# Kernel tuning notes

Measured on AMD Instinct MI355X. Metric: run time of the kernel, lower is better.

The kernel has to match this reference:

```python
import jax, jax.numpy as jnp
import numpy as np

# Module hyperparameters (match torch init_kwargs)
D_MODEL = 512
N_HEADS = 8
WINDOW_LEN = 128
DIL_FACTOR = 64
N_DIL = 2
ATTN_SINK = True
SRC_LEN = 2048
BSZ = 2


def setup_inputs() -> dict:
    key = jax.random.key(0)
    ks = jax.random.split(key, 6)
    w_scale = 0.04  # ~ xavier_uniform scale for 512x512
    inp = {
        "x": jax.random.normal(ks[0], (SRC_LEN, BSZ, D_MODEL), jnp.float32),
        "Wq": jax.random.normal(ks[1], (D_MODEL, D_MODEL), jnp.float32) * w_scale,
        "bq": jnp.zeros((D_MODEL,), jnp.float32),
        "Wk": jax.random.normal(ks[2], (D_MODEL, D_MODEL), jnp.float32) * w_scale,
        "bk": jnp.zeros((D_MODEL,), jnp.float32),
        "Wv": jax.random.normal(ks[3], (D_MODEL, D_MODEL), jnp.float32) * w_scale,
        "bv": jnp.zeros((D_MODEL,), jnp.float32),
        "Wo": jax.random.normal(ks[4], (D_MODEL, D_MODEL), jnp.float32) * w_scale,
        "bo": jnp.zeros((D_MODEL,), jnp.float32),
        "beta": jnp.zeros((N_HEADS,), jnp.float32),
    }
    return inp


def _fast_attention(x, Wq, bq, Wk, bk, Wv, bv, Wo, bo, beta):
    s, b, dm = x.shape  # (src_len, bsz, d_model)
    h = N_HEADS
    d = dm // h
    q = x @ Wq.T + bq
    k = x @ Wk.T + bk
    v = x @ Wv.T + bv

    def split_heads(t):  # 's b (h d) -> (b h) s d'
        return t.reshape(s, b, h, d).transpose(1, 2, 0, 3).reshape(b * h, s, d)

    q, k, v = split_heads(q), split_heads(k), split_heads(v)

    # beta: per-head temperature, tiled over batch (matches torch .repeat(bsz,1,1))
    beta_e = jnp.tile(jnp.exp(beta), b)[:, None, None]  # (b*h, 1, 1)
    q = q / (jnp.sqrt(jnp.asarray(d, q.dtype)) * beta_e)

    attn_out = jnp.zeros_like(v)
    z = b * h
    for i in range(N_DIL):
        dil = DIL_FACTOR ** i
        p = (WINDOW_LEN - 1) * dil
        pad = (p % s) if (p % s) != p else 0  # static python ints
        nw = pad // dil + 1  # num windows
        # causal left-padded strided windowed view of q: (z, nw, s, d)
        qp = jnp.pad(q, ((0, 0), (pad, 0), (0, 0)))
        idx = (jnp.arange(nw) * dil)[:, None] + jnp.arange(s)[None, :]  # (nw, s)
        qi = qp[:, idx, :]
        w = jnp.einsum('zbsd,zsd->zbs', qi, k)  # (z, nw, s)
        if ATTN_SINK:
            w = jnp.concatenate([w, jnp.zeros((z, 1, s), w.dtype)], axis=1)
        w = jax.nn.softmax(w, axis=1)  # softmax over window axis (+ sink)
        if ATTN_SINK:
            w = w[:, :-1]
        k2 = jnp.einsum('zbs,zsd->zbd', w, k)  # (z, nw, d)
        v2 = jnp.einsum('zbs,zsd->zbd', w, v)
        # left-pad back to full length (zeros at front, values at end)
        k = jnp.pad(k2, ((0, 0), (s - nw, 0), (0, 0)))
        v = jnp.pad(v2, ((0, 0), (s - nw, 0), (0, 0)))
        attn_out = attn_out + v

    # '(b h) s d -> s b (h d)'
    out = attn_out.reshape(b, h, s, d).transpose(2, 0, 1, 3).reshape(s, b, dm)
    return out @ Wo.T + bo


def reference(x, Wq, bq, Wk, bk, Wv, bv, Wo, bo, beta):
    return _fast_attention(x, Wq, bq, Wk, bk, Wv, bv, Wo, bo, beta)
```

## Files before the change

### kernel.cpp

```cpp
#include <hip/hip_runtime.h>
#include <hip/hip_bf16.h>
#include <math.h>

#define S_LEN 2048
#define BSZ 2
#define DM 512
#define NH 8
#define HD 64
#define RTOT (S_LEN*BSZ)
#define T_KEEP 32
#define ROW0 ((S_LEN - T_KEEP)*BSZ)
#define NXELEM (RTOT*DM)
#define NWROW  (NH*192)
#define NWELEM (NWROW*DM)

typedef __attribute__((ext_vector_type(8))) _Float16 half8;
typedef __attribute__((ext_vector_type(4))) float floatx4;

__device__ __forceinline__ short cvt1(float v) {
    _Float16 h = (_Float16)v;
    return __builtin_bit_cast(short, h);
}

__global__ __launch_bounds__(256) void convert(
    const float* __restrict__ x,
    const float* __restrict__ Wq, const float* __restrict__ Wk, const float* __restrict__ Wv,
    const float* __restrict__ bq, const float* __restrict__ bk, const float* __restrict__ bv,
    const float* __restrict__ bo,
    short* __restrict__ xf, short* __restrict__ wf, float* __restrict__ bcat,
    float* __restrict__ gbar, float* __restrict__ out)
{
    const int g = blockIdx.x*blockDim.x + threadIdx.x;
    const int stride = gridDim.x*blockDim.x;
    const int total4 = (NXELEM + NWELEM)/4;
    for (int i = g; i < total4; i += stride) {
        float4 v; size_t dst; short* d;
        if (i < NXELEM/4) {
            v = ((const float4*)x)[i];
            dst = (size_t)i*4; d = xf;
        } else {
            int j = i - NXELEM/4;
            int e = j*4;
            int R = e >> 9;
            int k = e & 511;
            int t = R >> 6;
            int hh = (t*683) >> 11;
            int m = t - 3*hh;
            int c = R & 63;
            const float* W = (m == 0 ? Wq : (m == 1 ? Wk : Wv));
            v = *(const float4*)&W[(size_t)(hh*HD + c)*DM + k];
            dst = (size_t)R*DM + k; d = wf;
        }
        short4 hv;
        hv.x = cvt1(v.x); hv.y = cvt1(v.y); hv.z = cvt1(v.z); hv.w = cvt1(v.w);
        *(short4*)&d[dst] = hv;
    }
    {
        const float4* b4 = (const float4*)bo;
        float4* o4 = (float4*)out;
        const int fill4 = ROW0*DM/4;
        for (int i = g; i < fill4; i += stride) o4[i] = b4[i & 127];
    }
    if (g < NWROW) {
        int t = g >> 6;
        int hh = (t*683) >> 11;
        int m = t - 3*hh;
        int c = g & 63;
        bcat[g] = (m == 0 ? bq : (m == 1 ? bk : bv))[hh*HD + c];
    }
    if (g < 2048) gbar[g] = 0.f;
}

__global__ __launch_bounds__(256) void qkv_gemm(
    const _Float16* __restrict__ xf, const _Float16* __restrict__ wf,
    const float* __restrict__ bcat, const float* __restrict__ beta,
    float* __restrict__ gbar, float* __restrict__ qsel)
{
    __shared__ __align__(16) float Cl[32*192];
    __shared__ float sb[256];

    const int tid  = threadIdx.x;
    const int w    = tid >> 6;
    const int lane = tid & 63;
    const int lrow = lane & 15;
    const int lk8  = lane >> 4;
    const int h    = blockIdx.y;
    const int r0   = blockIdx.x * 64;
    const int rowg = w >> 1;
    const int colg = w & 1;

    floatx4 acc[2][6];
    #pragma unroll
    for (int i = 0; i < 2; ++i)
        #pragma unroll
        for (int j = 0; j < 6; ++j) acc[i][j] = (floatx4)0.f;

    const _Float16* pA = xf + (size_t)(r0 + rowg*32 + lrow)*DM + lk8*8;
    const _Float16* pB = wf + (size_t)(h*192 + colg*96 + lrow)*DM + lk8*8;

    half8 Ab[2][2], Bb[2][6];
    #pragma unroll
    for (int i = 0; i < 2; ++i) Ab[0][i] = *(const half8*)(pA + (size_t)i*16*DM);
    #pragma unroll
    for (int j = 0; j < 6; ++j) Bb[0][j] = *(const half8*)(pB + (size_t)j*16*DM);

    #pragma unroll
    for (int kc = 0; kc < 16; ++kc) {
        const int buf = kc & 1;
        if (kc < 15) {
            const int nb = buf ^ 1;
            const int ko = (kc + 1)*32;
            #pragma unroll
            for (int i = 0; i < 2; ++i)
                Ab[nb][i] = *(const half8*)(pA + (size_t)i*16*DM + ko);
            #pragma unroll
            for (int j = 0; j < 6; ++j)
                Bb[nb][j] = *(const half8*)(pB + (size_t)j*16*DM + ko);
        }
        #pragma unroll
        for (int j = 0; j < 6; ++j)
            #pragma unroll
            for (int i = 0; i < 2; ++i)
                acc[i][j] = __builtin_amdgcn_mfma_f32_16x16x32_f16(Ab[buf][i], Bb[buf][j], acc[i][j], 0, 0, 0);
    }

    sb[tid] = 0.f;
    const float inv_scale = 1.0f / (8.0f * expf(beta[h]));
    float kacc0 = 0.f, kacc1 = 0.f, vacc0 = 0.f, vacc1 = 0.f;

    #pragma unroll
    for (int half = 0; half < 2; ++half) {
        __syncthreads();
        if (rowg == half) {
            #pragma unroll
            for (int i = 0; i < 2; ++i) {
                #pragma unroll
                for (int j = 0; j < 6; ++j) {
                    int col = colg*96 + j*16 + lrow;
                    float bias = bcat[h*192 + col];
                    #pragma unroll
                    for (int reg = 0; reg < 4; ++reg) {
                        int row = i*16 + lk8*4 + reg;
                        Cl[row*192 + col] = acc[i][j][reg] + bias;
                    }
                }
            }
        }
        __syncthreads();
        for (int i2 = w; i2 < 32; i2 += 4) {
            float qv = Cl[i2*192 + lane];
            float kv = Cl[i2*192 + 64 + lane];
            float vv = Cl[i2*192 + 128 + lane];
            int r = r0 + half*32 + i2;
            int s = r >> 1;
            int b = r & 1;
            if ((s & 63) == 63) {
                int wi = s >> 6;
                qsel[((size_t)(b*NH + h)*T_KEEP + wi)*64 + lane] = qv;
            }
            float p = qv * kv;
            #pragma unroll
            for (int off = 32; off > 0; off >>= 1) p += __shfl_xor(p, off, 64);
            float sig = 1.0f / (1.0f + expf(-p * inv_scale));
            if (b == 0) { kacc0 += sig*kv; vacc0 += sig*vv; }
            else        { kacc1 += sig*kv; vacc1 += sig*vv; }
        }
    }
    __syncthreads();

    atomicAdd(&sb[  0 + lane], kacc0);
    atomicAdd(&sb[ 64 + lane], vacc0);
    atomicAdd(&sb[128 + lane], kacc1);
    atomicAdd(&sb[192 + lane], vacc1);
    __syncthreads();
    {
        int b   = tid >> 7;
        int sel = (tid >> 6) & 1;
        int j   = tid & 63;
        int z   = b*NH + h;
        atomicAdd(&gbar[sel*1024 + z*64 + j], sb[tid]);
    }
}

__global__ __launch_bounds__(256) void headk(
    const float* __restrict__ qsel, const float* __restrict__ beta,
    const float* __restrict__ gbar, const float* __restrict__ Wo,
    float* __restrict__ coef, float* __restrict__ G)
{
    const int z = blockIdx.x;
    const int h = z & 7;
    const int tid = threadIdx.x;

    __shared__ float s_kb[64], s_vb[64];
    __shared__ float s_part[T_KEEP][8];
    __shared__ float s_gp[64][4];

    if (tid < 64) {
        s_kb[tid] = gbar[z*64 + tid];
        s_vb[tid] = gbar[1024 + z*64 + tid];
    }
    __syncthreads();

    {
        int wi = tid >> 3, jg = tid & 7;
        const float* qrow = &qsel[((size_t)z*T_KEEP + wi)*64 + jg*8];
        float4 q1 = *(const float4*)qrow;
        float4 q2 = *(const float4*)(qrow + 4);
        int j0 = jg*8;
        float p = q1.x*s_kb[j0] + q1.y*s_kb[j0+1] + q1.z*s_kb[j0+2] + q1.w*s_kb[j0+3]
                + q2.x*s_kb[j0+4] + q2.y*s_kb[j0+5] + q2.z*s_kb[j0+6] + q2.w*s_kb[j0+7];
        s_part[wi][jg] = p;
    }
    __syncthreads();
    if (tid < T_KEEP) {
        float sc = 0.f;
        #pragma unroll
        for (int gg = 0; gg < 8; ++gg) sc += s_part[tid][gg];
        sc *= 1.0f / (8.0f * expf(beta[h]));
        float m = sc;
        #pragma unroll
        for (int off = 16; off > 0; off >>= 1) m = fmaxf(m, __shfl_xor(m, off, 64));
        m = fmaxf(m, 0.f);
        float e = expf(sc - m);
        float d = e;
        #pragma unroll
        for (int off = 16; off > 0; off >>= 1) d += __shfl_xor(d, off, 64);
        d += expf(-m);
        float c = e / d;
        if (tid == T_KEEP-1) c += 1.0f;
        coef[z*T_KEEP + tid] = c;
    }

    const int cq = tid >> 2;
    const int jg = tid & 3;
    #pragma unroll
    for (int it = 0; it < 8; ++it) {
        int c = it*64 + cq;
        const float* wrow = &Wo[(size_t)c*DM + h*64 + jg*16];
        float a = 0.f;
        #pragma unroll
        for (int jj = 0; jj < 16; jj += 4) {
            float4 wv = *(const float4*)&wrow[jj];
            int j0 = jg*16 + jj;
            a += wv.x*s_vb[j0] + wv.y*s_vb[j0+1] + wv.z*s_vb[j0+2] + wv.w*s_vb[j0+3];
        }
        s_gp[cq][jg] = a;
        __syncthreads();
        if (tid < 64)
            G[(size_t)z*DM + it*64 + tid] = s_gp[tid][0] + s_gp[tid][1] + s_gp[tid][2] + s_gp[tid][3];
        __syncthreads();
    }
}

__global__ __launch_bounds__(256) void outk3(
    const float* __restrict__ coef, const float* __restrict__ G,
    const float* __restrict__ bo, float* __restrict__ out)
{
    const int a = blockIdx.x;
    const int b = a & 1;
    const int wi = a >> 1;
    const int tid = threadIdx.x;
    __shared__ float s_cf[NH];
    if (tid < NH) s_cf[tid] = coef[(b*NH + tid)*T_KEEP + wi];
    __syncthreads();
    for (int c = tid; c < DM; c += 256) {
        float v = bo[c];
        #pragma unroll
        for (int h = 0; h < NH; ++h)
            v += s_cf[h] * G[(size_t)(b*NH + h)*DM + c];
        out[(size_t)(ROW0 + a)*DM + c] = v;
    }
}

extern "C" void kernel_launch(void* const* d_in, const int* in_sizes, int n_in,
                              void* d_out, int out_size, void* d_ws, size_t ws_size,
                              hipStream_t stream) {
    const float* x    = (const float*)d_in[0];
    const float* Wq   = (const float*)d_in[1];
    const float* bq   = (const float*)d_in[2];
    const float* Wk   = (const float*)d_in[3];
    const float* bk   = (const float*)d_in[4];
    const float* Wv   = (const float*)d_in[5];
    const float* bv   = (const float*)d_in[6];
    const float* Wo   = (const float*)d_in[7];
    const float* bo   = (const float*)d_in[8];
    const float* beta = (const float*)d_in[9];

    char* ws = (char*)d_ws;
    float* gbar = (float*)(ws + 0);
    float* qsel = (float*)(ws + 8192);
    float* bcat = (float*)(ws + 139264);
    float* coef = (float*)(ws + 147456);
    float* G    = (float*)(ws + 149504);
    short* xf   = (short*)(ws + 182272);
    short* wf   = (short*)(ws + 182272 + 4194304);
    float* out  = (float*)d_out;

    convert<<<1024, 256, 0, stream>>>(x, Wq, Wk, Wv, bq, bk, bv, bo,
                                      xf, wf, bcat, gbar, out);
    dim3 g1(RTOT/64, NH);
    qkv_gemm<<<g1, 256, 0, stream>>>((const _Float16*)xf, (const _Float16*)wf,
                                     bcat, beta, gbar, qsel);
    headk<<<16, 256, 0, stream>>>(qsel, beta, gbar, Wo, coef, G);
    outk3<<<64, 256, 0, stream>>>(coef, G, bo, out);
}
```

Baseline: 132.6 us.

## Fuse head and output kernels, stage QKV GEMM tiles through LDS

Merges the per-head softmax-coefficient kernel and the output kernel into one kernel, outk4. It consumes a transposed copy of Wo prepared in the convert kernel and performs a 512x512 matvec per output row. The QKV GEMM now uses 32-row tiles with more blocks and occupancy hint 4, and loads A/B fragments through LDS via global_load_lds instead of register double-buffering. The aim is to remove one launch and raise GEMM occupancy. In exchange, each of the 64 output blocks re-reads the full WoT from cache, the strided transpose adds convert-kernel writes, and the single-buffered LDS loop adds barriers.

```diff
diff --git a/kernel.cpp b/kernel.cpp
--- a/kernel.cpp
+++ b/kernel.cpp
@@ -17,6 +17,11 @@
 typedef __attribute__((ext_vector_type(8))) _Float16 half8;
 typedef __attribute__((ext_vector_type(4))) float floatx4;
 
+__device__ __forceinline__ void gld16(const void* g, void* l) {
+    __builtin_amdgcn_global_load_lds((const __attribute__((address_space(1))) void*)g,
+                                     (__attribute__((address_space(3))) void*)l, 16, 0, 0);
+}
+
 __device__ __forceinline__ short cvt1(float v) {
     _Float16 h = (_Float16)v;
     return __builtin_bit_cast(short, h);
@@ -26,9 +31,9 @@
     const float* __restrict__ x,
     const float* __restrict__ Wq, const float* __restrict__ Wk, const float* __restrict__ Wv,
     const float* __restrict__ bq, const float* __restrict__ bk, const float* __restrict__ bv,
-    const float* __restrict__ bo,
+    const float* __restrict__ Wo, const float* __restrict__ bo,
     short* __restrict__ xf, short* __restrict__ wf, float* __restrict__ bcat,
-    float* __restrict__ gbar, float* __restrict__ out)
+    float* __restrict__ WoT, float* __restrict__ gbar, float* __restrict__ out)
 {
     const int g = blockIdx.x*blockDim.x + threadIdx.x;
     const int stride = gridDim.x*blockDim.x;
@@ -55,6 +60,15 @@
         hv.x = cvt1(v.x); hv.y = cvt1(v.y); hv.z = cvt1(v.z); hv.w = cvt1(v.w);
         *(short4*)&d[dst] = hv;
     }
+    for (int i = g; i < DM*DM/4; i += stride) {
+        int c  = i >> 7;
+        int k4 = (i & 127)*4;
+        float4 v = *(const float4*)&Wo[(size_t)c*DM + k4];
+        WoT[(size_t)(k4+0)*DM + c] = v.x;
+        WoT[(size_t)(k4+1)*DM + c] = v.y;
+        WoT[(size_t)(k4+2)*DM + c] = v.z;
+        WoT[(size_t)(k4+3)*DM + c] = v.w;
+    }
     {
         const float4* b4 = (const float4*)bo;
         float4* o4 = (float4*)out;
@@ -71,12 +85,12 @@
     if (g < 2048) gbar[g] = 0.f;
 }
 
-__global__ __launch_bounds__(256) void qkv_gemm(
+__global__ __launch_bounds__(256, 4) void qkv_gemm(
     const _Float16* __restrict__ xf, const _Float16* __restrict__ wf,
     const float* __restrict__ bcat, const float* __restrict__ beta,
     float* __restrict__ gbar, float* __restrict__ qsel)
 {
-    __shared__ __align__(16) float Cl[32*192];
+    __shared__ __align__(16) char smem[28672];
     __shared__ float sb[256];
 
     const int tid  = threadIdx.x;
@@ -85,86 +99,72 @@
     const int lrow = lane & 15;
     const int lk8  = lane >> 4;
     const int h    = blockIdx.y;
-    const int r0   = blockIdx.x * 64;
+    const int r0   = blockIdx.x * 32;
     const int rowg = w >> 1;
     const int colg = w & 1;
 
-    floatx4 acc[2][6];
+    floatx4 acc[6];
     #pragma unroll
-    for (int i = 0; i < 2; ++i)
-        #pragma unroll
-        for (int j = 0; j < 6; ++j) acc[i][j] = (floatx4)0.f;
-
-    const _Float16* pA = xf + (size_t)(r0 + rowg*32 + lrow)*DM + lk8*8;
-    const _Float16* pB = wf + (size_t)(h*192 + colg*96 + lrow)*DM + lk8*8;
-
-    half8 Ab[2][2], Bb[2][6];
+    for (int j = 0; j < 6; ++j) acc[j] = (floatx4)0.f;
+
+    const _Float16* asrc = xf + (size_t)(r0 + (w>>1)*16 + lrow)*DM + (w&1)*32 + lk8*8;
+    const _Float16* bsrc[6];
     #pragma unroll
-    for (int i = 0; i < 2; ++i) Ab[0][i] = *(const half8*)(pA + (size_t)i*16*DM);
+    for (int ii = 0; ii < 6; ++ii)
+        bsrc[ii] = wf + (size_t)(h*192 + (3*w + (ii>>1))*16 + lrow)*DM + (ii&1)*32 + lk8*8;
+
+    for (int kc = 0; kc < 8; ++kc) {
+        const int ko = kc*64;
+        gld16(asrc + ko, smem + w*1024);
+        #pragma unroll
+        for (int ii = 0; ii < 6; ++ii)
+            gld16(bsrc[ii] + ko, smem + 4096 + (6*w + ii)*1024);
+        __syncthreads();
+        #pragma unroll
+        for (int kh = 0; kh < 2; ++kh) {
+            half8 a = *(const half8*)(smem + (rowg*2 + kh)*1024 + lane*16);
+            #pragma unroll
+            for (int j = 0; j < 6; ++j) {
+                half8 b = *(const half8*)(smem + 4096 + ((colg*6 + j)*2 + kh)*1024 + lane*16);
+                acc[j] = __builtin_amdgcn_mfma_f32_16x16x32_f16(a, b, acc[j], 0, 0, 0);
+            }
+        }
+        __syncthreads();
+    }
+
+    float* Cl = (float*)smem;
     #pragma unroll
-    for (int j = 0; j < 6; ++j) Bb[0][j] = *(const half8*)(pB + (size_t)j*16*DM);
-
-    #pragma unroll
-    for (int kc = 0; kc < 16; ++kc) {
-        const int buf = kc & 1;
-        if (kc < 15) {
-            const int nb = buf ^ 1;
-            const int ko = (kc + 1)*32;
-            #pragma unroll
-            for (int i = 0; i < 2; ++i)
-                Ab[nb][i] = *(const half8*)(pA + (size_t)i*16*DM + ko);
-            #pragma unroll
-            for (int j = 0; j < 6; ++j)
-                Bb[nb][j] = *(const half8*)(pB + (size_t)j*16*DM + ko);
-        }
-        #pragma unroll
-        for (int j = 0; j < 6; ++j)
-            #pragma unroll
-            for (int i = 0; i < 2; ++i)
-                acc[i][j] = __builtin_amdgcn_mfma_f32_16x16x32_f16(Ab[buf][i], Bb[buf][j], acc[i][j], 0, 0, 0);
-    }
-
+    for (int j = 0; j < 6; ++j) {
+        int col = colg*96 + j*16 + lrow;
+        float bias = bcat[h*192 + col];
+        #pragma unroll
+        for (int reg = 0; reg < 4; ++reg) {
+            int row = rowg*16 + lk8*4 + reg;
+            Cl[row*192 + col] = acc[j][reg] + bias;
+        }
+    }
     sb[tid] = 0.f;
+    __syncthreads();
+
     const float inv_scale = 1.0f / (8.0f * expf(beta[h]));
     float kacc0 = 0.f, kacc1 = 0.f, vacc0 = 0.f, vacc1 = 0.f;
-
-    #pragma unroll
-    for (int half = 0; half < 2; ++half) {
-        __syncthreads();
-        if (rowg == half) {
-            #pragma unroll
-            for (int i = 0; i < 2; ++i) {
-                #pragma unroll
-                for (int j = 0; j < 6; ++j) {
-                    int col = colg*96 + j*16 + lrow;
-                    float bias = bcat[h*192 + col];
-                    #pragma unroll
-                    for (int reg = 0; reg < 4; ++reg) {
-                        int row = i*16 + lk8*4 + reg;
-                        Cl[row*192 + col] = acc[i][j][reg] + bias;
-                    }
-                }
-            }
-        }
-        __syncthreads();
-        for (int i2 = w; i2 < 32; i2 += 4) {
-            float qv = Cl[i2*192 + lane];
-            float kv = Cl[i2*192 + 64 + lane];
-            float vv = Cl[i2*192 + 128 + lane];
-            int r = r0 + half*32 + i2;
-            int s = r >> 1;
-            int b = r & 1;
-            if ((s & 63) == 63) {
-                int wi = s >> 6;
-                qsel[((size_t)(b*NH + h)*T_KEEP + wi)*64 + lane] = qv;
-            }
-            float p = qv * kv;
-            #pragma unroll
-            for (int off = 32; off > 0; off >>= 1) p += __shfl_xor(p, off, 64);
-            float sig = 1.0f / (1.0f + expf(-p * inv_scale));
-            if (b == 0) { kacc0 += sig*kv; vacc0 += sig*vv; }
-            else        { kacc1 += sig*kv; vacc1 += sig*vv; }
-        }
+    for (int i2 = w; i2 < 32; i2 += 4) {
+        float qv = Cl[i2*192 + lane];
+        float kv = Cl[i2*192 + 64 + lane];
+        float vv = Cl[i2*192 + 128 + lane];
+        int r = r0 + i2;
+        int s = r >> 1;
+        int b = r & 1;
+        if ((s & 63) == 63) {
+            int wi = s >> 6;
+            qsel[((size_t)(b*NH + h)*T_KEEP + wi)*64 + lane] = qv;
+        }
+        float p = qv * kv;
+        #pragma unroll
+        for (int off = 32; off > 0; off >>= 1) p += __shfl_xor(p, off, 64);
+        float sig = 1.0f / (1.0f + expf(-p * inv_scale));
+        if (b == 0) { kacc0 += sig*kv; vacc0 += sig*vv; }
+        else        { kacc1 += sig*kv; vacc1 += sig*vv; }
     }
     __syncthreads();
 
@@ -182,93 +182,75 @@
     }
 }
 
-__global__ __launch_bounds__(256) void headk(
+__global__ __launch_bounds__(256) void outk4(
     const float* __restrict__ qsel, const float* __restrict__ beta,
-    const float* __restrict__ gbar, const float* __restrict__ Wo,
-    float* __restrict__ coef, float* __restrict__ G)
-{
-    const int z = blockIdx.x;
-    const int h = z & 7;
-    const int tid = threadIdx.x;
-
-    __shared__ float s_kb[64], s_vb[64];
-    __shared__ float s_part[T_KEEP][8];
-    __shared__ float s_gp[64][4];
-
-    if (tid < 64) {
-        s_kb[tid] = gbar[z*64 + tid];
-        s_vb[tid] = gbar[1024 + z*64 + tid];
-    }
-    __syncthreads();
-
-    {
-        int wi = tid >> 3, jg = tid & 7;
-        const float* qrow = &qsel[((size_t)z*T_KEEP + wi)*64 + jg*8];
-        float4 q1 = *(const float4*)qrow;
-        float4 q2 = *(const float4*)(qrow + 4);
-        int j0 = jg*8;
-        float p = q1.x*s_kb[j0] + q1.y*s_kb[j0+1] + q1.z*s_kb[j0+2] + q1.w*s_kb[j0+3]
-                + q2.x*s_kb[j0+4] + q2.y*s_kb[j0+5] + q2.z*s_kb[j0+6] + q2.w*s_kb[j0+7];
-        s_part[wi][jg] = p;
-    }
-    __syncthreads();
-    if (tid < T_KEEP) {
-        float sc = 0.f;
-        #pragma unroll
-        for (int gg = 0; gg < 8; ++gg) sc += s_part[tid][gg];
-        sc *= 1.0f / (8.0f * expf(beta[h]));
-        float m = sc;
-        #pragma unroll
-        for (int off = 16; off > 0; off >>= 1) m = fmaxf(m, __shfl_xor(m, off, 64));
-        m = fmaxf(m, 0.f);
-        float e = expf(sc - m);
-        float d = e;
-        #pragma unroll
-        for (int off = 16; off > 0; off >>= 1) d += __shfl_xor(d, off, 64);
-        d += expf(-m);
-        float c = e / d;
-        if (tid == T_KEEP-1) c += 1.0f;
-        coef[z*T_KEEP + tid] = c;
-    }
-
-    const int cq = tid >> 2;
-    const int jg = tid & 3;
-    #pragma unroll
-    for (int it = 0; it < 8; ++it) {
-        int c = it*64 + cq;
-        const float* wrow = &Wo[(size_t)c*DM + h*64 + jg*16];
-        float a = 0.f;
-        #pragma unroll
-        for (int jj = 0; jj < 16; jj += 4) {
-            float4 wv = *(const float4*)&wrow[jj];
-            int j0 = jg*16 + jj;
-            a += wv.x*s_vb[j0] + wv.y*s_vb[j0+1] + wv.z*s_vb[j0+2] + wv.w*s_vb[j0+3];
-        }
-        s_gp[cq][jg] = a;
-        __syncthreads();
-        if (tid < 64)
-            G[(size_t)z*DM + it*64 + tid] = s_gp[tid][0] + s_gp[tid][1] + s_gp[tid][2] + s_gp[tid][3];
-        __syncthreads();
-    }
-}
-
-__global__ __launch_bounds__(256) void outk3(
-    const float* __restrict__ coef, const float* __restrict__ G,
+    const float* __restrict__ gbar, const float* __restrict__ WoT,
     const float* __restrict__ bo, float* __restrict__ out)
 {
     const int a = blockIdx.x;
     const int b = a & 1;
-    const int wi = a >> 1;
+    const int wi_blk = a >> 1;
     const int tid = threadIdx.x;
+
+    __shared__ float s_kb[512];
+    __shared__ float s_u[512];
     __shared__ float s_cf[NH];
-    if (tid < NH) s_cf[tid] = coef[(b*NH + tid)*T_KEEP + wi];
-    __syncthreads();
-    for (int c = tid; c < DM; c += 256) {
-        float v = bo[c];
-        #pragma unroll
-        for (int h = 0; h < NH; ++h)
-            v += s_cf[h] * G[(size_t)(b*NH + h)*DM + c];
-        out[(size_t)(ROW0 + a)*DM + c] = v;
+    __shared__ float s_part[512];
+
+    s_kb[tid]       = gbar[b*512 + tid];
+    s_kb[tid] = gbar[b*512 + tid];
+    s_part[tid]     = gbar[1024 + b*512 + tid];
+    s_part[tid+256] = gbar[1024 + b*512 + 256 + tid];
+    if (tid < 256) s_kb[tid+256] = gbar[b*512 + 256 + tid];
+    __syncthreads();
+
+    {
+        int h = tid >> 5, wi = tid & 31;
+        const float* qrow = &qsel[((size_t)(b*NH + h)*T_KEEP + wi)*64];
+        float sc = 0.f;
+        #pragma unroll
+        for (int j = 0; j < 64; j += 4) {
+            float4 q = *(const float4*)&qrow[j];
+            sc += q.x*s_kb[h*64+j] + q.y*s_kb[h*64+j+1] + q.z*s_kb[h*64+j+2] + q.w*s_kb[h*64+j+3];
+        }
+        sc *= 1.0f / (8.0f * expf(beta[h]));
+        float m = sc;
+        #pragma unroll
+        for (int off = 16; off > 0; off >>= 1) m = fmaxf(m, __shfl_xor(m, off, 32));
+        m = fmaxf(m, 0.f);
+        float e = expf(sc - m);
+        float d = e;
+        #pragma unroll
+        for (int off = 16; off > 0; off >>= 1) d += __shfl_xor(d, off, 32);
+        d += expf(-m);
+        if (wi == wi_blk) {
+            float c = e / d;
+            if (wi_blk == T_KEEP-1) c += 1.0f;
+            s_cf[h] = c;
+        }
+    }
+    __syncthreads();
+    s_u[tid]       = s_cf[tid >> 6]         * s_part[tid];
+    s_u[tid + 256] = s_cf[(tid + 256) >> 6] * s_part[tid + 256];
+    __syncthreads();
+
+    const int c0 = (tid & 127)*4;
+    const int kh = tid >> 7;
+    float4 accv = {0.f, 0.f, 0.f, 0.f};
+    for (int k = kh*256; k < kh*256 + 256; ++k) {
+        float u = s_u[k];
+        float4 wv = *(const float4*)&WoT[(size_t)k*DM + c0];
+        accv.x += u*wv.x; accv.y += u*wv.y; accv.z += u*wv.z; accv.w += u*wv.w;
+    }
+    __syncthreads();
+    if (kh == 1) *(float4*)&s_part[c0] = accv;
+    __syncthreads();
+    if (kh == 0) {
+        float4 pv = *(const float4*)&s_part[c0];
+        float4 bv = *(const float4*)&bo[c0];
+        accv.x += pv.x + bv.x; accv.y += pv.y + bv.y;
+        accv.z += pv.z + bv.z; accv.w += pv.w + bv.w;
+        *(float4*)&out[(size_t)(ROW0 + a)*DM + c0] = accv;
     }
 }
 
@@ -290,17 +272,15 @@
     float* gbar = (float*)(ws + 0);
     float* qsel = (float*)(ws + 8192);
     float* bcat = (float*)(ws + 139264);
-    float* coef = (float*)(ws + 147456);
-    float* G    = (float*)(ws + 149504);
-    short* xf   = (short*)(ws + 182272);
-    short* wf   = (short*)(ws + 182272 + 4194304);
+    float* WoT  = (float*)(ws + 147456);
+    short* xf   = (short*)(ws + 1196032);
+    short* wf   = (short*)(ws + 1196032 + 4194304);
     float* out  = (float*)d_out;
 
-    convert<<<1024, 256, 0, stream>>>(x, Wq, Wk, Wv, bq, bk, bv, bo,
-                                      xf, wf, bcat, gbar, out);
-    dim3 g1(RTOT/64, NH);
+    convert<<<1024, 256, 0, stream>>>(x, Wq, Wk, Wv, bq, bk, bv, Wo, bo,
+                                      xf, wf, bcat, WoT, gbar, out);
+    dim3 g1(RTOT/32, NH);
     qkv_gemm<<<g1, 256, 0, stream>>>((const _Float16*)xf, (const _Float16*)wf,
                                      bcat, beta, gbar, qsel);
-    headk<<<16, 256, 0, stream>>>(qsel, beta, gbar, Wo, coef, G);
-    outk3<<<64, 256, 0, stream>>>(coef, G, bo, out);
-}
+    outk4<<<64, 256, 0, stream>>>(qsel, beta, gbar, WoT, bo, out);
+}
```

Measured after the change: 137.9 us. +3.9%, slower.

## Shrink QKV GEMM tiles and stage operands through LDS via direct global-to-LDS loads

Applied to the files above, without the earlier changes.

The QKV GEMM block tile drops from 64 rows to 16 rows, so the grid has four times as many blocks. Each k-step now loads the A tile and twelve B tiles straight into shared memory with global_load_lds, and all four waves read the shared A fragment from there. Register use falls (3 accumulators instead of 12, with a 6-blocks-per-CU launch bound), which should raise occupancy and parallelism. The costs are that the same weight slice is re-read by four times as many blocks, there are two barriers per k-step, and the old register double-buffering is gone. The convert kernel's grid is also doubled.

```diff
diff --git a/kernel.cpp b/kernel.cpp
--- a/kernel.cpp
+++ b/kernel.cpp
@@ -16,6 +16,11 @@
 
 typedef __attribute__((ext_vector_type(8))) _Float16 half8;
 typedef __attribute__((ext_vector_type(4))) float floatx4;
+
+__device__ __forceinline__ void gld16(const void* g, void* l) {
+    __builtin_amdgcn_global_load_lds((const __attribute__((address_space(1))) void*)g,
+                                     (__attribute__((address_space(3))) void*)l, 16, 0, 0);
+}
 
 __device__ __forceinline__ short cvt1(float v) {
     _Float16 h = (_Float16)v;
@@ -71,12 +76,12 @@
     if (g < 2048) gbar[g] = 0.f;
 }
 
-__global__ __launch_bounds__(256) void qkv_gemm(
+__global__ __launch_bounds__(256, 6) void qkv_gemm(
     const _Float16* __restrict__ xf, const _Float16* __restrict__ wf,
     const float* __restrict__ bcat, const float* __restrict__ beta,
     float* __restrict__ gbar, float* __restrict__ qsel)
 {
-    __shared__ __align__(16) float Cl[32*192];
+    __shared__ __align__(16) char smem[13312];
     __shared__ float sb[256];
 
     const int tid  = threadIdx.x;
@@ -85,86 +90,70 @@
     const int lrow = lane & 15;
     const int lk8  = lane >> 4;
     const int h    = blockIdx.y;
-    const int r0   = blockIdx.x * 64;
-    const int rowg = w >> 1;
-    const int colg = w & 1;
-
-    floatx4 acc[2][6];
+    const int r0   = blockIdx.x * 16;
+
+    floatx4 acc[3];
     #pragma unroll
-    for (int i = 0; i < 2; ++i)
-        #pragma unroll
-        for (int j = 0; j < 6; ++j) acc[i][j] = (floatx4)0.f;
-
-    const _Float16* pA = xf + (size_t)(r0 + rowg*32 + lrow)*DM + lk8*8;
-    const _Float16* pB = wf + (size_t)(h*192 + colg*96 + lrow)*DM + lk8*8;
-
-    half8 Ab[2][2], Bb[2][6];
+    for (int j = 0; j < 3; ++j) acc[j] = (floatx4)0.f;
+
+    const _Float16* csrc[4];
+    int cdst[4];
+    int nch = 0;
+    for (int c = w; c < 13; c += 4) {
+        csrc[nch] = (c == 0)
+            ? xf + (size_t)(r0 + lrow)*DM + lk8*8
+            : wf + (size_t)(h*192 + (c-1)*16 + lrow)*DM + lk8*8;
+        cdst[nch] = c;
+        ++nch;
+    }
+
+    for (int kc = 0; kc < 16; ++kc) {
+        const int ko = kc*32;
+        for (int i = 0; i < nch; ++i)
+            gld16(csrc[i] + ko, smem + cdst[i]*1024);
+        __syncthreads();
+        half8 a = *(const half8*)(smem + lane*16);
+        #pragma unroll
+        for (int j = 0; j < 3; ++j) {
+            half8 b = *(const half8*)(smem + (1 + 3*w + j)*1024 + lane*16);
+            acc[j] = __builtin_amdgcn_mfma_f32_16x16x32_f16(a, b, acc[j], 0, 0, 0);
+        }
+        __syncthreads();
+    }
+
+    float* Cl = (float*)smem;
     #pragma unroll
-    for (int i = 0; i < 2; ++i) Ab[0][i] = *(const half8*)(pA + (size_t)i*16*DM);
-    #pragma unroll
-    for (int j = 0; j < 6; ++j) Bb[0][j] = *(const half8*)(pB + (size_t)j*16*DM);
-
-    #pragma unroll
-    for (int kc = 0; kc < 16; ++kc) {
-        const int buf = kc & 1;
-        if (kc < 15) {
-            const int nb = buf ^ 1;
-            const int ko = (kc + 1)*32;
-            #pragma unroll
-            for (int i = 0; i < 2; ++i)
-                Ab[nb][i] = *(const half8*)(pA + (size_t)i*16*DM + ko);
-            #pragma unroll
-            for (int j = 0; j < 6; ++j)
-                Bb[nb][j] = *(const half8*)(pB + (size_t)j*16*DM + ko);
-        }
-        #pragma unroll
-        for (int j = 0; j < 6; ++j)
-            #pragma unroll
-            for (int i = 0; i < 2; ++i)
-                acc[i][j] = __builtin_amdgcn_mfma_f32_16x16x32_f16(Ab[buf][i], Bb[buf][j], acc[i][j], 0, 0, 0);
-    }
-
+    for (int j = 0; j < 3; ++j) {
+        int col = w*48 + j*16 + lrow;
+        float bias = bcat[h*192 + col];
+        #pragma unroll
+        for (int reg = 0; reg < 4; ++reg) {
+            int row = lk8*4 + reg;
+            Cl[row*192 + col] = acc[j][reg] + bias;
+        }
+    }
     sb[tid] = 0.f;
+    __syncthreads();
+
     const float inv_scale = 1.0f / (8.0f * expf(beta[h]));
     float kacc0 = 0.f, kacc1 = 0.f, vacc0 = 0.f, vacc1 = 0.f;
-
-    #pragma unroll
-    for (int half = 0; half < 2; ++half) {
-        __syncthreads();
-        if (rowg == half) {
-            #pragma unroll
-            for (int i = 0; i < 2; ++i) {
-                #pragma unroll
-                for (int j = 0; j < 6; ++j) {
-                    int col = colg*96 + j*16 + lrow;
-                    float bias = bcat[h*192 + col];
-                    #pragma unroll
-                    for (int reg = 0; reg < 4; ++reg) {
-                        int row = i*16 + lk8*4 + reg;
-                        Cl[row*192 + col] = acc[i][j][reg] + bias;
-                    }
-                }
-            }
-        }
-        __syncthreads();
-        for (int i2 = w; i2 < 32; i2 += 4) {
-            float qv = Cl[i2*192 + lane];
-            float kv = Cl[i2*192 + 64 + lane];
-            float vv = Cl[i2*192 + 128 + lane];
-            int r = r0 + half*32 + i2;
-            int s = r >> 1;
-            int b = r & 1;
-            if ((s & 63) == 63) {
-                int wi = s >> 6;
-                qsel[((size_t)(b*NH + h)*T_KEEP + wi)*64 + lane] = qv;
-            }
-            float p = qv * kv;
-            #pragma unroll
-            for (int off = 32; off > 0; off >>= 1) p += __shfl_xor(p, off, 64);
-            float sig = 1.0f / (1.0f + expf(-p * inv_scale));
-            if (b == 0) { kacc0 += sig*kv; vacc0 += sig*vv; }
-            else        { kacc1 += sig*kv; vacc1 += sig*vv; }
-        }
+    for (int i2 = w; i2 < 16; i2 += 4) {
+        float qv = Cl[i2*192 + lane];
+        float kv = Cl[i2*192 + 64 + lane];
+        float vv = Cl[i2*192 + 128 + lane];
+        int r = r0 + i2;
+        int s = r >> 1;
+        int b = r & 1;
+        if ((s & 63) == 63) {
+            int wi = s >> 6;
+            qsel[((size_t)(b*NH + h)*T_KEEP + wi)*64 + lane] = qv;
+        }
+        float p = qv * kv;
+        #pragma unroll
+        for (int off = 32; off > 0; off >>= 1) p += __shfl_xor(p, off, 64);
+        float sig = 1.0f / (1.0f + expf(-p * inv_scale));
+        if (b == 0) { kacc0 += sig*kv; vacc0 += sig*vv; }
+        else        { kacc1 += sig*kv; vacc1 += sig*vv; }
     }
     __syncthreads();
 
@@ -296,9 +285,9 @@
     short* wf   = (short*)(ws + 182272 + 4194304);
     float* out  = (float*)d_out;
 
-    convert<<<1024, 256, 0, stream>>>(x, Wq, Wk, Wv, bq, bk, bv, bo,
+    convert<<<2048, 256, 0, stream>>>(x, Wq, Wk, Wv, bq, bk, bv, bo,
                                       xf, wf, bcat, gbar, out);
-    dim3 g1(RTOT/64, NH);
+    dim3 g1(RTOT/16, NH);
     qkv_gemm<<<g1, 256, 0, stream>>>((const _Float16*)xf, (const _Float16*)wf,
                                      bcat, beta, gbar, qsel);
     headk<<<16, 256, 0, stream>>>(qsel, beta, gbar, Wo, coef, G);
```

Result: slower. 155.8 us (+17.5%).
